# Kernel optimization log

Measured on AMD Instinct MI355X. Metric: run time of the kernel, lower is better.

## Reference

```python
import jax, jax.numpy as jnp
import numpy as np

N_NODES = 50000
N_EDGES = 800000
IN_DIM = 256
HID = 128


def setup_inputs() -> dict:
    key = jax.random.key(0)
    ks = jax.random.split(key, 8)
    x = jax.random.normal(ks[0], (N_NODES, IN_DIM), dtype=jnp.float32)
    edge_index = jax.random.randint(ks[1], (2, N_EDGES), 0, N_NODES, dtype=jnp.int32)
    edge_weight = jax.random.uniform(ks[2], (N_EDGES,), dtype=jnp.float32)
    # xavier_normal with gain=1.414 as in torch init
    g = 1.414
    W1 = jax.random.normal(ks[3], (HID, IN_DIM), dtype=jnp.float32) * (g * np.sqrt(2.0 / (HID + IN_DIM)))
    W2 = jax.random.normal(ks[4], (HID, HID), dtype=jnp.float32) * (g * np.sqrt(2.0 / (HID + HID)))
    b1 = jnp.zeros((HID,), dtype=jnp.float32)
    b2 = jnp.zeros((HID,), dtype=jnp.float32)
    a1 = jnp.full((1,), 0.25, dtype=jnp.float32)  # nn.PReLU() default init
    a2 = jnp.full((1,), 0.25, dtype=jnp.float32)
    return {"x": x, "edge_index": edge_index, "edge_weight": edge_weight,
            "W1": W1, "b1": b1, "a1": a1, "W2": W2, "b2": b2, "a2": a2}


def _gcn_layer(z, W, b, a, src, dst, w):
    # linear (no bias): [N, out]
    fts = z @ W.T
    # spmm: out[dst] += w * fts[src]
    msg = fts[src] * w[:, None]                      # [E, out]
    out = jax.ops.segment_sum(msg, dst, num_segments=N_NODES) + b
    # PReLU (single shared parameter)
    return jnp.where(out >= 0, out, a * out)


def reference(x, edge_index, edge_weight, W1, b1, a1, W2, b2, a2):
    src, dst = edge_index[0], edge_index[1]
    z = _gcn_layer(x, W1, b1, a1, src, dst, edge_weight)
    z = _gcn_layer(z, W2, b2, a2, src, dst, edge_weight)
    return z
```

## Files before the change

### kernel.cpp

```cpp
#include <hip/hip_runtime.h>
#include <hip/hip_bf16.h>

#define HID 128
#define BSH 6
#define BSZ 64
#define NBMAX 1024
#define HB 64
#define STAGE_BLKS 128

typedef unsigned int uint;
typedef unsigned short ushort;
typedef __attribute__((ext_vector_type(8))) short short8;
typedef __attribute__((ext_vector_type(4))) float f32x4;

__device__ __forceinline__ ushort bf16_of(float x) {
    return __bfloat16_as_ushort(__float2bfloat16(x));
}

__device__ __forceinline__ uint pack_bf16x2(float a, float b) {
    return (uint)bf16_of(a) | ((uint)bf16_of(b) << 16);
}

union FragAB { uint4 u; short8 s; };

__global__ __launch_bounds__(256) void pack_hist(
    const float* __restrict__ W1, const float* __restrict__ W2,
    ushort* __restrict__ Wb1, ushort* __restrict__ Wb2,
    const int* __restrict__ dst, int* __restrict__ hpart, int E, int NB) {
    int blk = blockIdx.x;
    if (blk >= 24) {
        __shared__ int h[NBMAX];
        int hb = blk - 24;
        for (int i = threadIdx.x; i < NB; i += 256) h[i] = 0;
        __syncthreads();
        int chunk = (E + HB - 1) / HB;
        int c0 = hb * chunk;
        int c1 = min(c0 + chunk, E);
        for (int e = c0 + threadIdx.x; e < c1; e += 256)
            atomicAdd(&h[dst[e] >> BSH], 1);
        __syncthreads();
        for (int i = threadIdx.x; i < NB; i += 256) hpart[hb * NBMAX + i] = h[i];
        return;
    }
    const float* W = (blk < 16) ? W1 : W2;
    ushort* Wb = (blk < 16) ? Wb1 : Wb2;
    int K = (blk < 16) ? 256 : 128;
    int t = ((blk < 16) ? blk : blk - 16) * 256 + threadIdx.x;
    int lane = t & 63, f = t >> 6;
    int s = f >> 3, c = f & 7;
    int m = c * 16 + (lane & 15);
    int k0 = s * 32 + (lane >> 4) * 8;
    const float* wr = W + (size_t)m * K + k0;
    float4 a = *(const float4*)wr;
    float4 b = *(const float4*)(wr + 4);
    uint4 o = make_uint4(pack_bf16x2(a.x, a.y), pack_bf16x2(a.z, a.w),
                         pack_bf16x2(b.x, b.y), pack_bf16x2(b.z, b.w));
    *(uint4*)(Wb + (size_t)t * 8) = o;
}

template <int K, bool ABF16>
__device__ __forceinline__ void gemm_body(
    const void* __restrict__ Xv, const ushort* __restrict__ Wb,
    ushort* __restrict__ out, int N, int bid) {
    const int lane = threadIdx.x & 63;
    const int wid  = threadIdx.x >> 6;
    const int n0   = bid * 64 + wid * 16;
    const int arow = n0 + (lane & 15);
    const bool ok  = arow < N;
    const int kgrp = (lane >> 4) * 8;
    const float*  xrow_f = (const float*)Xv + (size_t)arow * K;
    const ushort* xrow_h = (const ushort*)Xv + (size_t)arow * K;

    f32x4 acc[8];
#pragma unroll
    for (int c = 0; c < 8; ++c) acc[c] = (f32x4){0.f, 0.f, 0.f, 0.f};

#pragma unroll
    for (int s = 0; s < K / 32; ++s) {
        const int k0 = s * 32 + kgrp;
        FragAB af;
        if (ABF16) {
            af.u = ok ? *(const uint4*)(xrow_h + k0) : make_uint4(0, 0, 0, 0);
        } else {
            float4 va = make_float4(0.f, 0.f, 0.f, 0.f), vb = va;
            if (ok) {
                va = *(const float4*)(xrow_f + k0);
                vb = *(const float4*)(xrow_f + k0 + 4);
            }
            af.u = make_uint4(pack_bf16x2(va.x, va.y), pack_bf16x2(va.z, va.w),
                              pack_bf16x2(vb.x, vb.y), pack_bf16x2(vb.z, vb.w));
        }
#pragma unroll
        for (int c = 0; c < 8; ++c) {
            FragAB bfr;
            bfr.u = *(const uint4*)(Wb + (size_t)((s * 8 + c) * 64 + lane) * 8);
            acc[c] = __builtin_amdgcn_mfma_f32_16x16x32_bf16(af.s, bfr.s, acc[c], 0, 0, 0);
        }
    }
    const int col = lane & 15;
    const int rb = n0 + (lane >> 4) * 4;
#pragma unroll
    for (int c = 0; c < 8; ++c) {
#pragma unroll
        for (int r = 0; r < 4; ++r) {
            int n = rb + r;
            if (n < N) out[(size_t)n * HID + c * 16 + col] = bf16_of(acc[c][r]);
        }
    }
}

__device__ __forceinline__ void stage_body(
    const int* __restrict__ src, const int* __restrict__ dst,
    const float* __restrict__ w, int* __restrict__ gcur,
    int2* __restrict__ staged, int E, int NB, int bid) {
    __shared__ int lh[NBMAX], lb[NBMAX];
    for (int i = threadIdx.x; i < NB; i += 256) lh[i] = 0;
    __syncthreads();
    int chunk = (E + STAGE_BLKS - 1) / STAGE_BLKS;
    int c0 = bid * chunk;
    int c1 = min(c0 + chunk, E);
    for (int e = c0 + threadIdx.x; e < c1; e += 256)
        atomicAdd(&lh[dst[e] >> BSH], 1);
    __syncthreads();
    for (int i = threadIdx.x; i < NB; i += 256) {
        int c = lh[i];
        lb[i] = c ? atomicAdd(&gcur[i], c) : 0;
        lh[i] = 0;
    }
    __syncthreads();
    for (int e = c0 + threadIdx.x; e < c1; e += 256) {
        int d = dst[e];
        int b = d >> BSH;
        int slot = lb[b] + atomicAdd(&lh[b], 1);
        staged[slot] = make_int2(src[e] | ((d & (BSZ - 1)) << 16), __float_as_int(w[e]));
    }
}

__global__ __launch_bounds__(256) void gemm1_stage(
    const float* __restrict__ X, const ushort* __restrict__ Wb1,
    ushort* __restrict__ fts, int N, int gblk,
    const int* __restrict__ src, const int* __restrict__ dst,
    const float* __restrict__ w, int* __restrict__ gcur,
    int2* __restrict__ staged, int E, int NB) {
    int bid = blockIdx.x;
    if (bid < gblk) {
        gemm_body<256, false>(X, Wb1, fts, N, bid);
    } else {
        stage_body(src, dst, w, gcur, staged, E, NB, bid - gblk);
    }
}

template <int K, bool ABF16>
__global__ __launch_bounds__(256) void gemm_mfma(
    const void* __restrict__ Xv, const ushort* __restrict__ Wb,
    ushort* __restrict__ out, int N) {
    gemm_body<K, ABF16>(Xv, Wb, out, N, blockIdx.x);
}

__global__ __launch_bounds__(NBMAX) void bucket_scan(const int* __restrict__ hpart,
                                                     int* __restrict__ gbase,
                                                     int* __restrict__ gcur, int NB, int E) {
    __shared__ int l[NBMAX];
    int t = threadIdx.x;
    int v = 0;
    if (t < NB)
        for (int b = 0; b < HB; ++b) v += hpart[b * NBMAX + t];
    l[t] = v;
    __syncthreads();
    int x = v;
    for (int o = 1; o < NBMAX; o <<= 1) {
        int y = (t >= o) ? l[t - o] : 0;
        __syncthreads();
        x += y;
        l[t] = x;
        __syncthreads();
    }
    if (t < NB) { gbase[t] = x - v; gcur[t] = x - v; }
    if (t == 0) gbase[NB] = E;
}

__global__ __launch_bounds__(256) void node_sort(
    const int* __restrict__ gbase, const int2* __restrict__ staged,
    int2* __restrict__ csr, int* __restrict__ off, int N) {
    __shared__ int hist[BSZ];
    __shared__ int cur[BSZ];
    const int b = blockIdx.x;
    const int s0 = gbase[b], s1 = gbase[b + 1];
    const int t = threadIdx.x;
    if (t < BSZ) hist[t] = 0;
    __syncthreads();
    for (int e = s0 + t; e < s1; e += 256)
        atomicAdd(&hist[(staged[e].x >> 16) & (BSZ - 1)], 1);
    __syncthreads();
    if (t < BSZ) {
        int x = hist[t];
        int incl = x;
#pragma unroll
        for (int o = 1; o < BSZ; o <<= 1) {
            int y = __shfl_up(incl, o, BSZ);
            if (t >= o) incl += y;
        }
        int excl = incl - x;
        cur[t] = excl;
        int n = (b << BSH) + t;
        if (n <= N) off[n] = s0 + excl;
    }
    __syncthreads();
    for (int e = s0 + t; e < s1; e += 256) {
        int2 m = staged[e];
        int d = (m.x >> 16) & (BSZ - 1);
        int p = atomicAdd(&cur[d], 1);
        csr[s0 + p] = m;
    }
}

template <bool OUTBF16>
__global__ __launch_bounds__(256) void csr_gather_bf16(
    const int* __restrict__ off, const int2* __restrict__ edges,
    const ushort* __restrict__ fts, void* __restrict__ outv,
    const float* __restrict__ bias, const float* __restrict__ alpha, int N) {
    int d = blockIdx.x * 4 + (threadIdx.x >> 6);
    if (d >= N) return;
    const int lane = threadIdx.x & 63;
    const int g = lane >> 4;
    const int sub = lane & 15;
    int p = off[d];
    const int end = off[d + 1];
    float acc[8];
#pragma unroll
    for (int j = 0; j < 8; ++j) acc[j] = 0.f;

#define LOBITS(u_) __uint_as_float((u_) << 16)
#define HIBITS(u_) __uint_as_float((u_) & 0xffff0000u)
#define ROWOF(M_) (*(const uint4*)(fts + (size_t)((M_).x & 0xffff) * HID + sub * 8))
#define ACC8(R_, W_)                                              \
    do {                                                          \
        acc[0] += (W_) * LOBITS((R_).x); acc[1] += (W_) * HIBITS((R_).x); \
        acc[2] += (W_) * LOBITS((R_).y); acc[3] += (W_) * HIBITS((R_).y); \
        acc[4] += (W_) * LOBITS((R_).z); acc[5] += (W_) * HIBITS((R_).z); \
        acc[6] += (W_) * LOBITS((R_).w); acc[7] += (W_) * HIBITS((R_).w); \
    } while (0)

    for (; p + 16 <= end; p += 16) {
        int2 m0 = edges[p + g], m1 = edges[p + 4 + g];
        int2 m2 = edges[p + 8 + g], m3 = edges[p + 12 + g];
        uint4 r0 = ROWOF(m0), r1 = ROWOF(m1), r2 = ROWOF(m2), r3 = ROWOF(m3);
        float w0 = __int_as_float(m0.y), w1 = __int_as_float(m1.y);
        float w2 = __int_as_float(m2.y), w3 = __int_as_float(m3.y);
        ACC8(r0, w0); ACC8(r1, w1); ACC8(r2, w2); ACC8(r3, w3);
    }
    for (; p + 8 <= end; p += 8) {
        int2 ma = edges[p + g];
        int2 mb = edges[p + 4 + g];
        uint4 ra = ROWOF(ma), rb = ROWOF(mb);
        float wa = __int_as_float(ma.y), wb = __int_as_float(mb.y);
        ACC8(ra, wa);
        ACC8(rb, wb);
    }
    for (; p < end; p += 4) {
        int i = p + g;
        int2 m = edges[(i < end) ? i : (end - 1)];
        float wt = (i < end) ? __int_as_float(m.y) : 0.f;
        uint4 r = ROWOF(m);
        ACC8(r, wt);
    }
#undef ACC8
#undef ROWOF
#undef LOBITS
#undef HIBITS

#pragma unroll
    for (int j = 0; j < 8; ++j) {
        acc[j] += __shfl_xor(acc[j], 16);
        acc[j] += __shfl_xor(acc[j], 32);
    }

    const float a = alpha[0];
#pragma unroll
    for (int j = 0; j < 8; ++j) {
        float v = acc[j] + bias[sub * 8 + j];
        acc[j] = v >= 0.f ? v : a * v;
    }
    if (g == 0) {
        if (OUTBF16) {
            uint4 o = make_uint4(pack_bf16x2(acc[0], acc[1]), pack_bf16x2(acc[2], acc[3]),
                                 pack_bf16x2(acc[4], acc[5]), pack_bf16x2(acc[6], acc[7]));
            *(uint4*)((ushort*)outv + (size_t)d * HID + sub * 8) = o;
        } else {
            float* op = (float*)outv + (size_t)d * HID + sub * 8;
            *(float4*)op = make_float4(acc[0], acc[1], acc[2], acc[3]);
            *(float4*)(op + 4) = make_float4(acc[4], acc[5], acc[6], acc[7]);
        }
    }
}

extern "C" void kernel_launch(void* const* d_in, const int* in_sizes, int n_in,
                              void* d_out, int out_size, void* d_ws, size_t ws_size,
                              hipStream_t stream) {
    const float* x  = (const float*)d_in[0];
    const int*   ei = (const int*)d_in[1];
    const float* ew = (const float*)d_in[2];
    const float* W1 = (const float*)d_in[3];
    const float* b1 = (const float*)d_in[4];
    const float* a1 = (const float*)d_in[5];
    const float* W2 = (const float*)d_in[6];
    const float* b2 = (const float*)d_in[7];
    const float* a2 = (const float*)d_in[8];
    float* out = (float*)d_out;

    int N = in_sizes[0] / 256;
    int E = in_sizes[2];
    const int* src = ei;
    const int* dst = ei + E;
    int NB = (N + BSZ - 1) >> BSH;

    ushort* fts    = (ushort*)d_ws;
    ushort* agg    = fts + (size_t)N * HID;
    int2*   staged = (int2*)(agg + (size_t)N * HID);
    int2*   csr    = staged + E;
    ushort* Wb1    = (ushort*)(csr + E);
    ushort* Wb2    = Wb1 + 128 * 256;
    int*    hpart  = (int*)(Wb2 + 128 * 128);
    int*    gbase  = hpart + HB * NBMAX;
    int*    gcur   = gbase + NBMAX + 1;
    int*    off    = gcur + NBMAX;

    int gblk = (N + 63) / 64;
    int ggrid = (N + 3) / 4;

    pack_hist<<<24 + HB, 256, 0, stream>>>(W1, W2, Wb1, Wb2, dst, hpart, E, NB);
    bucket_scan<<<1, NBMAX, 0, stream>>>(hpart, gbase, gcur, NB, E);
    gemm1_stage<<<gblk + STAGE_BLKS, 256, 0, stream>>>(
        x, Wb1, fts, N, gblk, src, dst, ew, gcur, staged, E, NB);
    node_sort<<<NB, 256, 0, stream>>>(gbase, staged, csr, off, N);
    csr_gather_bf16<true><<<ggrid, 256, 0, stream>>>(off, csr, fts, agg, b1, a1, N);
    gemm_mfma<128, true><<<gblk, 256, 0, stream>>>(agg, Wb2, fts, N);
    csr_gather_bf16<false><<<ggrid, 256, 0, stream>>>(off, csr, fts, out, b2, a2, N);
}
```

Before: 142.7 us.

## Stage GEMM weight fragments in double-buffered LDS with register prefetch

The GEMM body now loads each k-step's packed bf16 weight fragments cooperatively into a double-buffered shared-memory tile. It prefetches the next step's weights and activation row into registers while the current step's MFMAs run. Out-of-range rows are clamped to the last row instead of being zero-masked, since only the stores are guarded. The aim is to cut redundant per-wave global weight loads and hide load latency, at the cost of a block-wide barrier every k-step and extra register pressure.

```diff
diff --git a/kernel.cpp b/kernel.cpp
--- a/kernel.cpp
+++ b/kernel.cpp
@@ -62,41 +62,65 @@
 __device__ __forceinline__ void gemm_body(
     const void* __restrict__ Xv, const ushort* __restrict__ Wb,
     ushort* __restrict__ out, int N, int bid) {
-    const int lane = threadIdx.x & 63;
-    const int wid  = threadIdx.x >> 6;
+    constexpr int NS = K / 32;
+    __shared__ uint4 Bs[2][512];
+    const int t    = threadIdx.x;
+    const int lane = t & 63;
+    const int wid  = t >> 6;
     const int n0   = bid * 64 + wid * 16;
-    const int arow = n0 + (lane & 15);
-    const bool ok  = arow < N;
+    const int arow = min(n0 + (lane & 15), N - 1);
     const int kgrp = (lane >> 4) * 8;
-    const float*  xrow_f = (const float*)Xv + (size_t)arow * K;
-    const ushort* xrow_h = (const ushort*)Xv + (size_t)arow * K;
+    const float*  xrow_f = (const float*)Xv + (size_t)arow * K + kgrp;
+    const ushort* xrow_h = (const ushort*)Xv + (size_t)arow * K + kgrp;
+    const uint4* Wbv = (const uint4*)Wb;
+
+    uint4 b0 = Wbv[t];
+    uint4 b1 = Wbv[256 + t];
+    float4 va, vb;
+    uint4 ha;
+    if (ABF16) ha = *(const uint4*)xrow_h;
+    else { va = *(const float4*)xrow_f; vb = *(const float4*)(xrow_f + 4); }
+    Bs[0][t] = b0;
+    Bs[0][256 + t] = b1;
+    __syncthreads();
 
     f32x4 acc[8];
 #pragma unroll
     for (int c = 0; c < 8; ++c) acc[c] = (f32x4){0.f, 0.f, 0.f, 0.f};
 
 #pragma unroll
-    for (int s = 0; s < K / 32; ++s) {
-        const int k0 = s * 32 + kgrp;
+    for (int s = 0; s < NS; ++s) {
+        const int cur = s & 1;
+        uint4 nb0, nb1;
+        float4 nva, nvb;
+        uint4 nha;
+        if (s + 1 < NS) {
+            nb0 = Wbv[(s + 1) * 512 + t];
+            nb1 = Wbv[(s + 1) * 512 + 256 + t];
+            if (ABF16) nha = *(const uint4*)(xrow_h + (s + 1) * 32);
+            else {
+                nva = *(const float4*)(xrow_f + (s + 1) * 32);
+                nvb = *(const float4*)(xrow_f + (s + 1) * 32 + 4);
+            }
+        }
         FragAB af;
-        if (ABF16) {
-            af.u = ok ? *(const uint4*)(xrow_h + k0) : make_uint4(0, 0, 0, 0);
-        } else {
-            float4 va = make_float4(0.f, 0.f, 0.f, 0.f), vb = va;
-            if (ok) {
-                va = *(const float4*)(xrow_f + k0);
-                vb = *(const float4*)(xrow_f + k0 + 4);
-            }
-            af.u = make_uint4(pack_bf16x2(va.x, va.y), pack_bf16x2(va.z, va.w),
-                              pack_bf16x2(vb.x, vb.y), pack_bf16x2(vb.z, vb.w));
-        }
+        if (ABF16) af.u = ha;
+        else af.u = make_uint4(pack_bf16x2(va.x, va.y), pack_bf16x2(va.z, va.w),
+                               pack_bf16x2(vb.x, vb.y), pack_bf16x2(vb.z, vb.w));
 #pragma unroll
         for (int c = 0; c < 8; ++c) {
             FragAB bfr;
-            bfr.u = *(const uint4*)(Wb + (size_t)((s * 8 + c) * 64 + lane) * 8);
+            bfr.u = Bs[cur][c * 64 + lane];
             acc[c] = __builtin_amdgcn_mfma_f32_16x16x32_bf16(af.s, bfr.s, acc[c], 0, 0, 0);
         }
-    }
+        if (s + 1 < NS) {
+            Bs[cur ^ 1][t] = nb0;
+            Bs[cur ^ 1][256 + t] = nb1;
+            ha = nha; va = nva; vb = nvb;
+        }
+        __syncthreads();
+    }
+
     const int col = lane & 15;
     const int rb = n0 + (lane >> 4) * 4;
 #pragma unroll
```

Measured after the change: 140.2 us. Within noise of the previous version (-1.7%).
